# Performance work log

Measured on AMD Instinct MI355X. Metric: run time of the kernel, lower is better.

Reference implementation:

```python
import jax, jax.numpy as jnp
import numpy as np

N_NODES = 100000
N_EDGES = 1600000
N_CLASS = 26
HIDDEN = 128
K = 3  # TAGConv hops


def setup_inputs() -> dict:
    key = jax.random.key(0)
    ks = jax.random.split(key, 12)
    x = jax.random.normal(ks[0], (N_NODES, N_CLASS), dtype=jnp.float32)
    edge_index = jax.random.randint(ks[1], (2, N_EDGES), 0, N_NODES, dtype=jnp.int64)
    edge_weight = jax.random.uniform(ks[2], (N_EDGES,), dtype=jnp.float32)
    # Per-hop weights (K+1 hops incl. hop 0) for each of the 3 TAGConv layers.
    def lin(k, fan_in, fan_out):
        s = 1.0 / np.sqrt(fan_in)
        return jax.random.uniform(k, (K + 1, fan_in, fan_out), dtype=jnp.float32, minval=-s, maxval=s)
    W1 = lin(ks[3], N_CLASS, HIDDEN)
    b1 = jnp.zeros((HIDDEN,), dtype=jnp.float32)
    W2 = lin(ks[4], HIDDEN, HIDDEN)
    b2 = jnp.zeros((HIDDEN,), dtype=jnp.float32)
    W3 = lin(ks[5], HIDDEN, N_CLASS)
    b3 = jnp.zeros((N_CLASS,), dtype=jnp.float32)
    return {"x": x, "edge_index": edge_index, "edge_weight": edge_weight,
            "W1": W1, "b1": b1, "W2": W2, "b2": b2, "W3": W3, "b3": b3}


def _gcn_norm(edge_index, edge_weight, n):
    # symmetric normalization deg^-1/2 * w * deg^-1/2, no self loops (PyG TAGConv)
    row, col = edge_index[0], edge_index[1]
    deg = jax.ops.segment_sum(edge_weight, col, num_segments=n)
    dinv = jnp.where(deg > 0, jax.lax.rsqrt(jnp.maximum(deg, 1e-12)), 0.0)
    return dinv[row] * edge_weight * dinv[col]


def _tag_conv(x, row, col, norm, W, b, n):
    # out = sum_k W_k(x_k), x_0 = x, x_k = A_norm x_{k-1}
    out = x @ W[0]
    h = x
    for k in range(1, K + 1):
        h = jax.ops.segment_sum(norm[:, None] * h[row], col, num_segments=n)
        out = out + h @ W[k]
    return out + b


def reference(x, edge_index, edge_weight, W1, b1, W2, b2, W3, b3):
    n = x.shape[0]
    row, col = edge_index[0], edge_index[1]
    norm = _gcn_norm(edge_index, edge_weight, n)  # identical for all 3 layers
    h = jax.nn.elu(_tag_conv(x, row, col, norm, W1, b1, n))
    h = jax.nn.elu(_tag_conv(h, row, col, norm, W2, b2, n))
    return _tag_conv(h, row, col, norm, W3, b3, n)
```

## Files before the change

### kernel.cpp

```cpp
#include <hip/hip_runtime.h>

#define NCLS 26
#define HID 128
#define EPB 8192
#define MAXBK 512
#define BCAP 6016
typedef unsigned short ushort_t;
typedef unsigned int uint_t;
typedef unsigned long long u64;

typedef __bf16 bf16x8 __attribute__((ext_vector_type(8)));
typedef float f32x4 __attribute__((ext_vector_type(4)));
typedef unsigned int u32x4 __attribute__((ext_vector_type(4)));
typedef unsigned int u32x2 __attribute__((ext_vector_type(2)));

static __device__ __forceinline__ float b2f(ushort_t h) {
  return __uint_as_float(((uint_t)h) << 16);
}
static __device__ __forceinline__ ushort_t f2b(float f) {
  uint_t u = __float_as_uint(f);
  uint_t r = (u + 0x7fffu + ((u >> 16) & 1u)) >> 16;
  return (ushort_t)r;
}
static __device__ __forceinline__ uint_t pack2(float f0, float f1) {
  return (uint_t)f2b(f0) | ((uint_t)f2b(f1) << 16);
}
static __device__ __forceinline__ float lo16(uint_t v) { return b2f((ushort_t)(v & 0xffffu)); }
static __device__ __forceinline__ float hi16(uint_t v) { return b2f((ushort_t)(v >> 16)); }
static __device__ __forceinline__ bf16x8 ld_frag(const ushort_t* p) {
  u32x4 v = *reinterpret_cast<const u32x4*>(p);
  return __builtin_bit_cast(bf16x8, v);
}


__global__ __launch_bounds__(256) void bucket_place(
    const int* __restrict__ ei, const float* __restrict__ ew,
    int* __restrict__ gcur, u64* __restrict__ bkt, int E, int nbk) {
  __shared__ uint_t lc[MAXBK];
  __shared__ uint_t lb[MAXBK];
  int tid = threadIdx.x;
  for (int t = tid; t < nbk; t += 256) lc[t] = 0;
  __syncthreads();
  int e0 = blockIdx.x * EPB;
#pragma unroll
  for (int i = 0; i < EPB / 256; ++i) {
    int e = e0 + tid + i * 256;
    if (e < E) atomicAdd(&lc[(uint_t)ei[E + e] >> 8], 1u);
  }
  __syncthreads();
  for (int t = tid; t < nbk; t += 256) {
    uint_t c = lc[t];
    lb[t] = c ? (uint_t)t * BCAP + (uint_t)atomicAdd(&gcur[t], (int)c) : 0u;
    lc[t] = 0;
  }
  __syncthreads();
#pragma unroll
  for (int i = 0; i < EPB / 256; ++i) {
    int e = e0 + tid + i * 256;
    if (e < E) {
      uint_t r = (uint_t)ei[e];
      uint_t c = (uint_t)ei[E + e];
      uint_t b = c >> 8;
      uint_t pos = lb[b] + atomicAdd(&lc[b], 1u);
      bkt[pos] = ((u64)(r | ((c & 255u) << 24)) << 32) | (u64)__float_as_uint(ew[e]);
    }
  }
}

__global__ void scan_buckets(const int* __restrict__ gcur, int* __restrict__ mbase,
                             int nbk, int E) {
  __shared__ int s[512];
  int t = threadIdx.x;
  int v = (t < nbk) ? gcur[t] : 0;
  s[t] = v;
  __syncthreads();
  for (int off = 1; off < 512; off <<= 1) {
    int u = (t >= off) ? s[t - off] : 0;
    __syncthreads();
    s[t] += u;
    __syncthreads();
  }
  if (t < nbk) mbase[t] = s[t] - v;
  if (t == 0) mbase[nbk] = E;
}

__global__ __launch_bounds__(256) void bucket_stats(
    const u64* __restrict__ bkt, const int* __restrict__ gcur, const int* __restrict__ mbase,
    int* __restrict__ start, float* __restrict__ dinv, int n, int E) {
  int b = blockIdx.x;
  __shared__ uint_t cnt[256];
  __shared__ float deg[256];
  __shared__ int ssc[256];
  int tid = threadIdx.x;
  cnt[tid] = 0;
  deg[tid] = 0.f;
  __syncthreads();
  int fill = gcur[b];
  const u64* w = bkt + (size_t)b * BCAP;
  for (int p = tid; p < fill; p += 256) {
    u64 v = w[p];
    uint_t cl = (uint_t)(v >> 56);
    float wv = __uint_as_float((uint_t)(v & 0xffffffffULL));
    atomicAdd(&cnt[cl], 1u);
    atomicAdd(&deg[cl], wv);
  }
  __syncthreads();
  int v0 = (int)cnt[tid];
  ssc[tid] = v0;
  __syncthreads();
  for (int off = 1; off < 256; off <<= 1) {
    int u = (tid >= off) ? ssc[tid - off] : 0;
    __syncthreads();
    ssc[tid] += u;
    __syncthreads();
  }
  int node = (b << 8) + tid;
  if (node < n) {
    start[node] = mbase[b] + ssc[tid] - v0;
    float d = deg[tid];
    dinv[node] = d > 0.f ? rsqrtf(fmaxf(d, 1e-12f)) : 0.f;
  }
  if (b == 0 && tid == 0) start[n] = E;
}

__global__ __launch_bounds__(256) void bucket_emit(
    const u64* __restrict__ bkt, const int* __restrict__ gcur, const int* __restrict__ start,
    const float* __restrict__ dinv, u32x2* __restrict__ meta, int n) {
  int b = blockIdx.x;
  __shared__ uint_t lcur[256];
  int tid = threadIdx.x;
  lcur[tid] = 0;
  __syncthreads();
  int fill = gcur[b];
  const u64* w = bkt + (size_t)b * BCAP;
  for (int p = tid; p < fill; p += 256) {
    u64 v = w[p];
    uint_t hi = (uint_t)(v >> 32);
    uint_t r = hi & 0xffffffu;
    uint_t cl = hi >> 24;
    float wv = __uint_as_float((uint_t)(v & 0xffffffffULL));
    uint_t node = ((uint_t)b << 8) + cl;
    float nrm = dinv[r] * wv * dinv[node];
    uint_t slot = (uint_t)start[node] + atomicAdd(&lcur[cl], 1u);
    u32x2 m;
    m.x = r;
    m.y = __float_as_uint(nrm);
    meta[slot] = m;
  }
}

__global__ __launch_bounds__(256) void prep_misc(
    const float* __restrict__ x, uint_t* __restrict__ x32,
    const float* __restrict__ W1, ushort_t* __restrict__ Wz1,
    const float* __restrict__ W2, ushort_t* __restrict__ Wz2,
    const float* __restrict__ W3, ushort_t* __restrict__ Wz3, int n, int gconv) {
  int blk = blockIdx.x;
  int tid = threadIdx.x;
  if (blk < gconv) {
    int idx = blk * 256 + tid;
    if (idx >= n * 16) return;
    int node = idx >> 4, lane = idx & 15;
    float f0 = 0.f, f1 = 0.f;
    if (lane < 13) {
      f0 = x[node * 26 + 2 * lane];
      f1 = x[node * 26 + 2 * lane + 1];
    }
    x32[idx] = pack2(f0, f1);
  } else if (blk < gconv + 64) {
    int idx = (blk - gconv) * 256 + tid;
    int i = idx & 7, l = (idx >> 3) & 63, j = (idx >> 9) & 7, t = idx >> 12;
    int k = 8 * (l >> 4) + i;
    int col = 16 * j + (l & 15);
    float v = (k < NCLS) ? W1[((size_t)t * NCLS + k) * 128 + col] : 0.f;
    Wz1[idx] = f2b(v);
  } else if (blk < gconv + 64 + 256) {
    int idx = (blk - gconv - 64) * 256 + tid;
    int i = idx & 7, l = (idx >> 3) & 63, j = (idx >> 9) & 7, t = idx >> 12;
    int s = t >> 2, tt = t & 3;
    int k = tt * 32 + 8 * (l >> 4) + i;
    int col = 16 * j + (l & 15);
    float v = W2[((size_t)s * HID + k) * 128 + col];
    Wz2[idx] = f2b(v);
  } else {
    int idx = (blk - gconv - 64 - 256) * 256 + tid;
    int i = idx & 7, l = (idx >> 3) & 63, j = (idx >> 9) & 7, t = idx >> 12;
    int k = t * 32 + 8 * (l >> 4) + i;
    int col = 16 * j + (l & 15);
    int s = col >> 5, c = col & 31;
    float v = (c < 26) ? W3[((size_t)s * 128 + k) * 26 + c] : 0.f;
    Wz3[idx] = f2b(v);
  }
}


__global__ __launch_bounds__(256) void spmm128_bf(
    const u32x2* __restrict__ meta, const int* __restrict__ start,
    const uint_t* __restrict__ in, uint_t* __restrict__ out, int n) {
  int node = blockIdx.x * 4 + (threadIdx.x >> 6);
  int lane = threadIdx.x & 63;
  if (node >= n) return;
  int s = start[node], m = start[node + 1] - s;
  int eq = lane >> 4;
  uint_t foff = (uint_t)(lane & 15) << 4;
  const char* inb = (const char*)in;
  float a0 = 0.f, a1 = 0.f, a2 = 0.f, a3 = 0.f, a4 = 0.f, a5 = 0.f, a6 = 0.f, a7 = 0.f;
  if (m > 0) {
    int i0 = eq, i1 = 4 + eq;
    u32x2 mt0 = meta[s + (i0 < m ? i0 : m - 1)];
    u32x2 mt1 = meta[s + (i1 < m ? i1 : m - 1)];
    for (int base = 0; base < m; base += 8) {
      int p0 = base + 8 + eq, p1 = base + 12 + eq;
      u32x2 nx0 = meta[s + (p0 < m ? p0 : m - 1)];
      u32x2 nx1 = meta[s + (p1 < m ? p1 : m - 1)];
      float w0 = (base + eq < m) ? __uint_as_float(mt0.y) : 0.f;
      float w1 = (base + 4 + eq < m) ? __uint_as_float(mt1.y) : 0.f;
      u32x4 v0 = *reinterpret_cast<const u32x4*>(inb + (((uint_t)mt0.x << 8) + foff));
      u32x4 v1 = *reinterpret_cast<const u32x4*>(inb + (((uint_t)mt1.x << 8) + foff));
      a0 += w0 * lo16(v0.x); a1 += w0 * hi16(v0.x);
      a2 += w0 * lo16(v0.y); a3 += w0 * hi16(v0.y);
      a4 += w0 * lo16(v0.z); a5 += w0 * hi16(v0.z);
      a6 += w0 * lo16(v0.w); a7 += w0 * hi16(v0.w);
      a0 += w1 * lo16(v1.x); a1 += w1 * hi16(v1.x);
      a2 += w1 * lo16(v1.y); a3 += w1 * hi16(v1.y);
      a4 += w1 * lo16(v1.z); a5 += w1 * hi16(v1.z);
      a6 += w1 * lo16(v1.w); a7 += w1 * hi16(v1.w);
      mt0 = nx0;
      mt1 = nx1;
    }
  }
  a0 += __shfl_xor(a0, 16); a1 += __shfl_xor(a1, 16);
  a2 += __shfl_xor(a2, 16); a3 += __shfl_xor(a3, 16);
  a4 += __shfl_xor(a4, 16); a5 += __shfl_xor(a5, 16);
  a6 += __shfl_xor(a6, 16); a7 += __shfl_xor(a7, 16);
  a0 += __shfl_xor(a0, 32); a1 += __shfl_xor(a1, 32);
  a2 += __shfl_xor(a2, 32); a3 += __shfl_xor(a3, 32);
  a4 += __shfl_xor(a4, 32); a5 += __shfl_xor(a5, 32);
  a6 += __shfl_xor(a6, 32); a7 += __shfl_xor(a7, 32);
  if (eq == 0) {
    u32x4 o;
    o.x = pack2(a0, a1);
    o.y = pack2(a2, a3);
    o.z = pack2(a4, a5);
    o.w = pack2(a6, a7);
    *reinterpret_cast<u32x4*>(out + (size_t)node * 64 + (foff >> 2)) = o;
  }
}

__global__ __launch_bounds__(256) void spmm26_bf(
    const u32x2* __restrict__ meta, const int* __restrict__ start,
    const uint_t* __restrict__ in, const uint_t* __restrict__ add,
    uint_t* __restrict__ out, int n) {
  int node = blockIdx.x * 32 + (threadIdx.x >> 3);
  int ln = threadIdx.x & 7;
  if (node >= n) return;
  int s = start[node], m = start[node + 1] - s;
  uint_t foff = (uint_t)ln << 3;
  const char* inb = (const char*)in;
  float a0 = 0.f, a1 = 0.f, a2 = 0.f, a3 = 0.f;
  if (m > 0) {
    for (int base = 0; base < m; base += 8) {
      int j = base + ln;
      u32x2 mt = meta[s + (j < m ? j : m - 1)];
      int rr = (int)mt.x;
      float ww = (j < m) ? __uint_as_float(mt.y) : 0.f;
#pragma unroll
      for (int k = 0; k < 8; ++k) {
        uint_t r = (uint_t)__shfl(rr, k, 8);
        float wv = __shfl(ww, k, 8);
        u32x2 v = *reinterpret_cast<const u32x2*>(inb + ((r << 6) + foff));
        a0 += wv * lo16(v.x); a1 += wv * hi16(v.x);
        a2 += wv * lo16(v.y); a3 += wv * hi16(v.y);
      }
    }
  }
  if (add) {
    u32x2 v = *reinterpret_cast<const u32x2*>(add + (size_t)node * 16 + 2 * ln);
    a0 += lo16(v.x); a1 += hi16(v.x);
    a2 += lo16(v.y); a3 += hi16(v.y);
  }
  u32x2 o;
  o.x = pack2(a0, a1);
  o.y = pack2(a2, a3);
  *reinterpret_cast<u32x2*>(out + (size_t)node * 16 + 2 * ln) = o;
}

__global__ __launch_bounds__(256) void spmm26_addf(
    const u32x2* __restrict__ meta, const int* __restrict__ start,
    const uint_t* __restrict__ in, float* __restrict__ out, int n) {
  int node = blockIdx.x * 32 + (threadIdx.x >> 3);
  int ln = threadIdx.x & 7;
  if (node >= n) return;
  int s = start[node], m = start[node + 1] - s;
  uint_t foff = (uint_t)ln << 3;
  const char* inb = (const char*)in;
  float a0 = 0.f, a1 = 0.f, a2 = 0.f, a3 = 0.f;
  if (m > 0) {
    for (int base = 0; base < m; base += 8) {
      int j = base + ln;
      u32x2 mt = meta[s + (j < m ? j : m - 1)];
      int rr = (int)mt.x;
      float ww = (j < m) ? __uint_as_float(mt.y) : 0.f;
#pragma unroll
      for (int k = 0; k < 8; ++k) {
        uint_t r = (uint_t)__shfl(rr, k, 8);
        float wv = __shfl(ww, k, 8);
        u32x2 v = *reinterpret_cast<const u32x2*>(inb + ((r << 6) + foff));
        a0 += wv * lo16(v.x); a1 += wv * hi16(v.x);
        a2 += wv * lo16(v.y); a3 += wv * hi16(v.y);
      }
    }
  }
  int c0 = 4 * ln;
  if (c0 + 0 < 26) out[(size_t)node * 26 + c0 + 0] += a0;
  if (c0 + 1 < 26) out[(size_t)node * 26 + c0 + 1] += a1;
  if (c0 + 2 < 26) out[(size_t)node * 26 + c0 + 2] += a2;
  if (c0 + 3 < 26) out[(size_t)node * 26 + c0 + 3] += a3;
}

template <int KW, int NSRC, int EPI, int GROUP>
__global__ __launch_bounds__(256) void mfma_gemm(
    const ushort_t* __restrict__ A0, const ushort_t* __restrict__ A1,
    const ushort_t* __restrict__ A2, const ushort_t* __restrict__ A3,
    const ushort_t* __restrict__ Wswz, const float* __restrict__ bias,
    ushort_t* __restrict__ outb, float* __restrict__ outf, int n) {
  constexpr int KSPS = KW / 32;
  constexpr int KSTEPS = NSRC * KSPS;
  constexpr int NGROUPS = KSTEPS / GROUP;
  __shared__ ushort_t sW[GROUP * 4096];
  const int tid = threadIdx.x;
  const int w = tid >> 6;
  const int l = tid & 63;
  const int row0 = blockIdx.x * 64 + w * 16;
  const int koff = 8 * (l >> 4);
  const int arow = row0 + (l & 15);
  const int arow_c = arow < n ? arow : (n - 1);

  f32x4 acc[8];
#pragma unroll
  for (int j = 0; j < 8; ++j) acc[j] = (f32x4){0.f, 0.f, 0.f, 0.f};

  const ushort_t* const srcs[4] = {A0, A1, A2, A3};

  auto aload = [&](int t) {
    const int s = t / KSPS;
    const int tt = t - s * KSPS;
    return ld_frag(srcs[s] + (size_t)arow_c * KW + tt * 32 + koff);
  };

  bf16x8 afA[GROUP], afB[GROUP];
#pragma unroll
  for (int c = 0; c < GROUP; ++c) afA[c] = aload(c);
  u32x4 gw[2 * GROUP];
#pragma unroll
  for (int c = 0; c < GROUP; ++c) {
    const ushort_t* p = Wswz + (size_t)c * 4096 + tid * 8;
    gw[2 * c] = *reinterpret_cast<const u32x4*>(p);
    gw[2 * c + 1] = *reinterpret_cast<const u32x4*>(p + 2048);
  }

#pragma unroll
  for (int g = 0; g < NGROUPS; ++g) {
    __syncthreads();
#pragma unroll
    for (int c = 0; c < GROUP; ++c) {
      *reinterpret_cast<u32x4*>(sW + c * 4096 + tid * 8) = gw[2 * c];
      *reinterpret_cast<u32x4*>(sW + c * 4096 + tid * 8 + 2048) = gw[2 * c + 1];
    }
    if (g + 1 < NGROUPS) {
#pragma unroll
      for (int c = 0; c < GROUP; ++c) {
        const ushort_t* p = Wswz + (size_t)(g + 1) * GROUP * 4096 + (size_t)c * 4096 + tid * 8;
        gw[2 * c] = *reinterpret_cast<const u32x4*>(p);
        gw[2 * c + 1] = *reinterpret_cast<const u32x4*>(p + 2048);
      }
#pragma unroll
      for (int c = 0; c < GROUP; ++c) {
        if (g & 1)
          afA[c] = aload((g + 1) * GROUP + c);
        else
          afB[c] = aload((g + 1) * GROUP + c);
      }
    }
    __syncthreads();
#pragma unroll
    for (int tg = 0; tg < GROUP; ++tg) {
      bf16x8 af = (g & 1) ? afB[tg] : afA[tg];
      const ushort_t* wp = sW + tg * 4096 + l * 8;
#pragma unroll
      for (int j = 0; j < 8; ++j) {
        bf16x8 bfr = ld_frag(wp + j * 64 * 8);
        acc[j] = __builtin_amdgcn_mfma_f32_16x16x32_bf16(af, bfr, acc[j], 0, 0, 0);
      }
    }
  }

  const int ccol = l & 15;
  const int crow0 = row0 + 4 * (l >> 4);
#pragma unroll
  for (int j = 0; j < 8; ++j) {
    if (EPI == 0) {
      int col = 16 * j + ccol;
      float bi = bias[col];
#pragma unroll
      for (int r = 0; r < 4; ++r) {
        int row = crow0 + r;
        if (row >= n) continue;
        float v = acc[j][r] + bi;
        v = v > 0.f ? v : (__expf(v) - 1.f);
        outb[(size_t)row * 128 + col] = f2b(v);
      }
    } else {
      int slot = j >> 1;
      int c = 16 * (j & 1) + ccol;
#pragma unroll
      for (int r = 0; r < 4; ++r) {
        int row = crow0 + r;
        if (row >= n) continue;
        float v = acc[j][r];
        if (slot == 0) {
          if (c < 26) outf[(size_t)row * 26 + c] = v + bias[c];
        } else {
          outb[((size_t)(slot - 1) * n + row) * 32 + c] = f2b(v);
        }
      }
    }
  }
}


extern "C" void kernel_launch(void* const* d_in, const int* in_sizes, int n_in,
                              void* d_out, int out_size, void* d_ws, size_t ws_size,
                              hipStream_t stream) {
  const float* x  = (const float*)d_in[0];
  const int*   ei = (const int*)d_in[1];
  const float* ew = (const float*)d_in[2];
  const float* W1 = (const float*)d_in[3];
  const float* b1 = (const float*)d_in[4];
  const float* W2 = (const float*)d_in[5];
  const float* b2 = (const float*)d_in[6];
  const float* W3 = (const float*)d_in[7];
  const float* b3 = (const float*)d_in[8];
  float* out = (float*)d_out;

  const int n = in_sizes[0] / NCLS;
  const int E = in_sizes[2];
  const int nbk = (n + 255) >> 8;

  char* w = (char*)d_ws;
  auto alloc = [&](size_t bytes) {
    char* p = w;
    w += (bytes + 255) / 256 * 256;
    return p;
  };
  uint_t* H0 = (uint_t*)alloc((size_t)n * 64 * 4);
  uint_t* P1 = (uint_t*)alloc((size_t)n * 64 * 4);
  uint_t* P2 = (uint_t*)alloc((size_t)n * 64 * 4);
  uint_t* P3 = (uint_t*)alloc((size_t)n * 64 * 4);
  uint_t* H1 = (uint_t*)alloc((size_t)n * 64 * 4);
  uint_t* x32 = (uint_t*)alloc((size_t)n * 16 * 4);
  uint_t* q1  = (uint_t*)alloc((size_t)n * 16 * 4);
  uint_t* q2  = (uint_t*)alloc((size_t)n * 16 * 4);
  uint_t* q3  = (uint_t*)alloc((size_t)n * 16 * 4);
  uint_t* zb  = (uint_t*)alloc((size_t)n * 48 * 4);
  ushort_t* Wz1 = (ushort_t*)alloc(4 * 4096 * 2);
  ushort_t* Wz2 = (ushort_t*)alloc(16 * 4096 * 2);
  ushort_t* Wz3 = (ushort_t*)alloc(4 * 4096 * 2);
  u64*   bkt  = (u64*)zb;
  u32x2* meta = (u32x2*)alloc((size_t)E * 8);
  int*   start = (int*)alloc((size_t)(n + 1) * 4);
  float* dinv  = (float*)alloc((size_t)n * 4);
  int*   gcur  = (int*)alloc(MAXBK * 4);
  int*   mbase = (int*)alloc((MAXBK + 1) * 4);

  const int ab = (E + EPB - 1) / EPB;
  const int gconv = (n * 16 + 255) / 256;

  prep_misc<<<gconv + 64 + 256 + 64, 256, 0, stream>>>(x, x32, W1, Wz1, W2, Wz2, W3, Wz3,
                                                       n, gconv);

  hipMemsetAsync(gcur, 0, MAXBK * 4, stream);
  bucket_place<<<ab, 256, 0, stream>>>(ei, ew, gcur, bkt, E, nbk);
  scan_buckets<<<1, 512, 0, stream>>>(gcur, mbase, nbk, E);
  bucket_stats<<<nbk, 256, 0, stream>>>(bkt, gcur, mbase, start, dinv, n, E);
  bucket_emit<<<nbk, 256, 0, stream>>>(bkt, gcur, start, dinv, meta, n);

  const int g128 = (n + 3) / 4;
  const int g26  = (n + 31) / 32;
  const int gg   = (n + 63) / 64;

  spmm26_bf<<<g26, 256, 0, stream>>>(meta, start, x32, nullptr, q1, n);
  spmm26_bf<<<g26, 256, 0, stream>>>(meta, start, q1, nullptr, q2, n);
  spmm26_bf<<<g26, 256, 0, stream>>>(meta, start, q2, nullptr, q3, n);
  mfma_gemm<32, 4, 0, 4><<<gg, 256, 0, stream>>>(
      (const ushort_t*)x32, (const ushort_t*)q1, (const ushort_t*)q2, (const ushort_t*)q3,
      Wz1, b1, (ushort_t*)H0, nullptr, n);

  spmm128_bf<<<g128, 256, 0, stream>>>(meta, start, H0, P1, n);
  spmm128_bf<<<g128, 256, 0, stream>>>(meta, start, P1, P2, n);
  spmm128_bf<<<g128, 256, 0, stream>>>(meta, start, P2, P3, n);
  mfma_gemm<128, 4, 0, 4><<<gg, 256, 0, stream>>>(
      (const ushort_t*)H0, (const ushort_t*)P1, (const ushort_t*)P2, (const ushort_t*)P3,
      Wz2, b2, (ushort_t*)H1, nullptr, n);

  mfma_gemm<128, 1, 1, 4><<<gg, 256, 0, stream>>>(
      (const ushort_t*)H1, (const ushort_t*)H1, (const ushort_t*)H1, (const ushort_t*)H1,
      Wz3, b3, (ushort_t*)zb, out, n);

  uint_t* z1 = zb;
  uint_t* z2 = zb + (size_t)n * 16;
  uint_t* z3 = zb + (size_t)n * 32;
  spmm26_bf<<<g26, 256, 0, stream>>>(meta, start, z3, z2, q1, n);
  spmm26_bf<<<g26, 256, 0, stream>>>(meta, start, q1, z1, q2, n);
  spmm26_addf<<<g26, 256, 0, stream>>>(meta, start, q2, out, n);
}
```

Before: 458.1 us.

## Slice feature matrices into 16-column planes and pack edge metadata into 32 bits

Stores all node-feature matrices as column slices of 16 bf16 values, so each row slice is 32 bytes, and rewrites the SpMM kernels so each block handles one slice for a group of nodes, processing two nodes per wavefront. Edge metadata is compressed to a single 32-bit word: a 17-bit source index plus a 15-bit bf16 weight with the sign bit dropped. The GEMM loads and epilogues are updated to read and write the sliced layout. The aim is to improve cache locality of the random gathers, since each slice pass touches a smaller working set, and to halve metadata traffic. The cost is lower weight precision, a node count limited to 17 bits, and metadata being re-read once per slice.

```diff
diff --git a/kernel.cpp b/kernel.cpp
--- a/kernel.cpp
+++ b/kernel.cpp
@@ -125,7 +125,7 @@
 
 __global__ __launch_bounds__(256) void bucket_emit(
     const u64* __restrict__ bkt, const int* __restrict__ gcur, const int* __restrict__ start,
-    const float* __restrict__ dinv, u32x2* __restrict__ meta, int n) {
+    const float* __restrict__ dinv, uint_t* __restrict__ meta, int n) {
   int b = blockIdx.x;
   __shared__ uint_t lcur[256];
   int tid = threadIdx.x;
@@ -142,10 +142,7 @@
     uint_t node = ((uint_t)b << 8) + cl;
     float nrm = dinv[r] * wv * dinv[node];
     uint_t slot = (uint_t)start[node] + atomicAdd(&lcur[cl], 1u);
-    u32x2 m;
-    m.x = r;
-    m.y = __float_as_uint(nrm);
-    meta[slot] = m;
+    meta[slot] = (((uint_t)f2b(nrm) & 0x7FFFu) << 17) | r;
   }
 }
 
@@ -165,7 +162,7 @@
       f0 = x[node * 26 + 2 * lane];
       f1 = x[node * 26 + 2 * lane + 1];
     }
-    x32[idx] = pack2(f0, f1);
+    x32[((size_t)(lane >> 3) * n + node) * 8 + (lane & 7)] = pack2(f0, f1);
   } else if (blk < gconv + 64) {
     int idx = (blk - gconv) * 256 + tid;
     int i = idx & 7, l = (idx >> 3) & 63, j = (idx >> 9) & 7, t = idx >> 12;
@@ -192,129 +189,122 @@
   }
 }
 
-
-__global__ __launch_bounds__(256) void spmm128_bf(
-    const u32x2* __restrict__ meta, const int* __restrict__ start,
-    const uint_t* __restrict__ in, uint_t* __restrict__ out, int n) {
-  int node = blockIdx.x * 4 + (threadIdx.x >> 6);
-  int lane = threadIdx.x & 63;
-  if (node >= n) return;
-  int s = start[node], m = start[node + 1] - s;
-  int eq = lane >> 4;
-  uint_t foff = (uint_t)(lane & 15) << 4;
-  const char* inb = (const char*)in;
-  float a0 = 0.f, a1 = 0.f, a2 = 0.f, a3 = 0.f, a4 = 0.f, a5 = 0.f, a6 = 0.f, a7 = 0.f;
-  if (m > 0) {
-    int i0 = eq, i1 = 4 + eq;
-    u32x2 mt0 = meta[s + (i0 < m ? i0 : m - 1)];
-    u32x2 mt1 = meta[s + (i1 < m ? i1 : m - 1)];
-    for (int base = 0; base < m; base += 8) {
-      int p0 = base + 8 + eq, p1 = base + 12 + eq;
-      u32x2 nx0 = meta[s + (p0 < m ? p0 : m - 1)];
-      u32x2 nx1 = meta[s + (p1 < m ? p1 : m - 1)];
-      float w0 = (base + eq < m) ? __uint_as_float(mt0.y) : 0.f;
-      float w1 = (base + 4 + eq < m) ? __uint_as_float(mt1.y) : 0.f;
-      u32x4 v0 = *reinterpret_cast<const u32x4*>(inb + (((uint_t)mt0.x << 8) + foff));
-      u32x4 v1 = *reinterpret_cast<const u32x4*>(inb + (((uint_t)mt1.x << 8) + foff));
-      a0 += w0 * lo16(v0.x); a1 += w0 * hi16(v0.x);
-      a2 += w0 * lo16(v0.y); a3 += w0 * hi16(v0.y);
-      a4 += w0 * lo16(v0.z); a5 += w0 * hi16(v0.z);
-      a6 += w0 * lo16(v0.w); a7 += w0 * hi16(v0.w);
-      a0 += w1 * lo16(v1.x); a1 += w1 * hi16(v1.x);
-      a2 += w1 * lo16(v1.y); a3 += w1 * hi16(v1.y);
-      a4 += w1 * lo16(v1.z); a5 += w1 * hi16(v1.z);
-      a6 += w1 * lo16(v1.w); a7 += w1 * hi16(v1.w);
-      mt0 = nx0;
-      mt1 = nx1;
-    }
-  }
-  a0 += __shfl_xor(a0, 16); a1 += __shfl_xor(a1, 16);
-  a2 += __shfl_xor(a2, 16); a3 += __shfl_xor(a3, 16);
-  a4 += __shfl_xor(a4, 16); a5 += __shfl_xor(a5, 16);
-  a6 += __shfl_xor(a6, 16); a7 += __shfl_xor(a7, 16);
-  a0 += __shfl_xor(a0, 32); a1 += __shfl_xor(a1, 32);
-  a2 += __shfl_xor(a2, 32); a3 += __shfl_xor(a3, 32);
-  a4 += __shfl_xor(a4, 32); a5 += __shfl_xor(a5, 32);
-  a6 += __shfl_xor(a6, 32); a7 += __shfl_xor(a7, 32);
-  if (eq == 0) {
-    u32x4 o;
-    o.x = pack2(a0, a1);
-    o.y = pack2(a2, a3);
-    o.z = pack2(a4, a5);
-    o.w = pack2(a6, a7);
-    *reinterpret_cast<u32x4*>(out + (size_t)node * 64 + (foff >> 2)) = o;
-  }
-}
-
-__global__ __launch_bounds__(256) void spmm26_bf(
-    const u32x2* __restrict__ meta, const int* __restrict__ start,
+template <int NSLOG, int NPW>
+__global__ __launch_bounds__(256) void spmm_sl(
+    const uint_t* __restrict__ umeta, const int* __restrict__ start,
     const uint_t* __restrict__ in, const uint_t* __restrict__ add,
     uint_t* __restrict__ out, int n) {
-  int node = blockIdx.x * 32 + (threadIdx.x >> 3);
-  int ln = threadIdx.x & 7;
-  if (node >= n) return;
-  int s = start[node], m = start[node + 1] - s;
-  uint_t foff = (uint_t)ln << 3;
-  const char* inb = (const char*)in;
-  float a0 = 0.f, a1 = 0.f, a2 = 0.f, a3 = 0.f;
-  if (m > 0) {
-    for (int base = 0; base < m; base += 8) {
-      int j = base + ln;
-      u32x2 mt = meta[s + (j < m ? j : m - 1)];
-      int rr = (int)mt.x;
-      float ww = (j < m) ? __uint_as_float(mt.y) : 0.f;
-#pragma unroll
-      for (int k = 0; k < 8; ++k) {
-        uint_t r = (uint_t)__shfl(rr, k, 8);
-        float wv = __shfl(ww, k, 8);
-        u32x2 v = *reinterpret_cast<const u32x2*>(inb + ((r << 6) + foff));
-        a0 += wv * lo16(v.x); a1 += wv * hi16(v.x);
-        a2 += wv * lo16(v.y); a3 += wv * hi16(v.y);
-      }
-    }
-  }
-  if (add) {
-    u32x2 v = *reinterpret_cast<const u32x2*>(add + (size_t)node * 16 + 2 * ln);
-    a0 += lo16(v.x); a1 += hi16(v.x);
-    a2 += lo16(v.y); a3 += hi16(v.y);
-  }
-  u32x2 o;
-  o.x = pack2(a0, a1);
-  o.y = pack2(a2, a3);
-  *reinterpret_cast<u32x2*>(out + (size_t)node * 16 + 2 * ln) = o;
-}
-
-__global__ __launch_bounds__(256) void spmm26_addf(
-    const u32x2* __restrict__ meta, const int* __restrict__ start,
+  constexpr int NS = 1 << NSLOG;
+  const int bid = blockIdx.x;
+  const int sl = bid & (NS - 1);
+  const int wid = threadIdx.x >> 6;
+  const int lane = threadIdx.x & 63;
+  const int eg = lane >> 2, fl = lane & 3;
+  const size_t slb = (size_t)sl * ((size_t)n * 8);
+  const uint_t* inS = in + slb;
+  const int node0 = (bid >> NSLOG) * (4 * NPW) + wid * NPW;
+
+#pragma unroll
+  for (int nn = 0; nn < NPW; nn += 2) {
+    int nodeA = node0 + nn;
+    int nodeB = node0 + nn + 1;
+    if (nodeA >= n) return;
+    bool hasB = nodeB < n;
+    int sA = start[nodeA], mA = start[nodeA + 1] - sA;
+    int sB = hasB ? start[nodeB] : sA;
+    int mB = hasB ? start[nodeB + 1] - sB : 0;
+    float a0 = 0.f, a1 = 0.f, a2 = 0.f, a3 = 0.f;
+    float b0 = 0.f, b1 = 0.f, b2 = 0.f, b3 = 0.f;
+    int mmax = mA > mB ? mA : mB;
+    for (int base = 0; base < mmax; base += 16) {
+      int e = base + eg;
+      int ciA = e < mA ? e : (mA > 0 ? mA - 1 : 0);
+      int ciB = e < mB ? e : (mB > 0 ? mB - 1 : 0);
+      uint_t mvA = umeta[sA + ciA];
+      uint_t mvB = umeta[sB + ciB];
+      float wA = (e < mA) ? __uint_as_float((mvA >> 17) << 16) : 0.f;
+      float wB = (e < mB) ? __uint_as_float((mvB >> 17) << 16) : 0.f;
+      u32x2 vA = *reinterpret_cast<const u32x2*>(inS + (mvA & 0x1FFFFu) * 8 + fl * 2);
+      u32x2 vB = *reinterpret_cast<const u32x2*>(inS + (mvB & 0x1FFFFu) * 8 + fl * 2);
+      a0 += wA * lo16(vA.x); a1 += wA * hi16(vA.x);
+      a2 += wA * lo16(vA.y); a3 += wA * hi16(vA.y);
+      b0 += wB * lo16(vB.x); b1 += wB * hi16(vB.x);
+      b2 += wB * lo16(vB.y); b3 += wB * hi16(vB.y);
+    }
+#pragma unroll
+    for (int st = 4; st <= 32; st <<= 1) {
+      a0 += __shfl_xor(a0, st); a1 += __shfl_xor(a1, st);
+      a2 += __shfl_xor(a2, st); a3 += __shfl_xor(a3, st);
+      b0 += __shfl_xor(b0, st); b1 += __shfl_xor(b1, st);
+      b2 += __shfl_xor(b2, st); b3 += __shfl_xor(b3, st);
+    }
+    if (lane < 4) {
+      size_t oA = slb + (size_t)nodeA * 8 + fl * 2;
+      if (add) {
+        u32x2 av = *reinterpret_cast<const u32x2*>(add + oA);
+        a0 += lo16(av.x); a1 += hi16(av.x);
+        a2 += lo16(av.y); a3 += hi16(av.y);
+      }
+      u32x2 ov;
+      ov.x = pack2(a0, a1);
+      ov.y = pack2(a2, a3);
+      *reinterpret_cast<u32x2*>(out + oA) = ov;
+      if (hasB) {
+        size_t oB = slb + (size_t)nodeB * 8 + fl * 2;
+        if (add) {
+          u32x2 av = *reinterpret_cast<const u32x2*>(add + oB);
+          b0 += lo16(av.x); b1 += hi16(av.x);
+          b2 += lo16(av.y); b3 += hi16(av.y);
+        }
+        u32x2 ov2;
+        ov2.x = pack2(b0, b1);
+        ov2.y = pack2(b2, b3);
+        *reinterpret_cast<u32x2*>(out + oB) = ov2;
+      }
+    }
+  }
+}
+
+template <int NPW>
+__global__ __launch_bounds__(256) void spmm_addf_sl(
+    const uint_t* __restrict__ umeta, const int* __restrict__ start,
     const uint_t* __restrict__ in, float* __restrict__ out, int n) {
-  int node = blockIdx.x * 32 + (threadIdx.x >> 3);
-  int ln = threadIdx.x & 7;
-  if (node >= n) return;
-  int s = start[node], m = start[node + 1] - s;
-  uint_t foff = (uint_t)ln << 3;
-  const char* inb = (const char*)in;
-  float a0 = 0.f, a1 = 0.f, a2 = 0.f, a3 = 0.f;
-  if (m > 0) {
-    for (int base = 0; base < m; base += 8) {
-      int j = base + ln;
-      u32x2 mt = meta[s + (j < m ? j : m - 1)];
-      int rr = (int)mt.x;
-      float ww = (j < m) ? __uint_as_float(mt.y) : 0.f;
-#pragma unroll
-      for (int k = 0; k < 8; ++k) {
-        uint_t r = (uint_t)__shfl(rr, k, 8);
-        float wv = __shfl(ww, k, 8);
-        u32x2 v = *reinterpret_cast<const u32x2*>(inb + ((r << 6) + foff));
-        a0 += wv * lo16(v.x); a1 += wv * hi16(v.x);
-        a2 += wv * lo16(v.y); a3 += wv * hi16(v.y);
-      }
-    }
-  }
-  int c0 = 4 * ln;
-  if (c0 + 0 < 26) out[(size_t)node * 26 + c0 + 0] += a0;
-  if (c0 + 1 < 26) out[(size_t)node * 26 + c0 + 1] += a1;
-  if (c0 + 2 < 26) out[(size_t)node * 26 + c0 + 2] += a2;
-  if (c0 + 3 < 26) out[(size_t)node * 26 + c0 + 3] += a3;
+  const int bid = blockIdx.x;
+  const int sl = bid & 1;
+  const int wid = threadIdx.x >> 6;
+  const int lane = threadIdx.x & 63;
+  const int eg = lane >> 2, fl = lane & 3;
+  const size_t slb = (size_t)sl * ((size_t)n * 8);
+  const uint_t* inS = in + slb;
+  const int node0 = (bid >> 1) * (4 * NPW) + wid * NPW;
+
+#pragma unroll
+  for (int nn = 0; nn < NPW; ++nn) {
+    int node = node0 + nn;
+    if (node >= n) return;
+    int s = start[node], m = start[node + 1] - s;
+    float a0 = 0.f, a1 = 0.f, a2 = 0.f, a3 = 0.f;
+    for (int base = 0; base < m; base += 16) {
+      int e = base + eg;
+      uint_t mv = umeta[s + (e < m ? e : m - 1)];
+      float w = (e < m) ? __uint_as_float((mv >> 17) << 16) : 0.f;
+      u32x2 v = *reinterpret_cast<const u32x2*>(inS + (mv & 0x1FFFFu) * 8 + fl * 2);
+      a0 += w * lo16(v.x); a1 += w * hi16(v.x);
+      a2 += w * lo16(v.y); a3 += w * hi16(v.y);
+    }
+#pragma unroll
+    for (int st = 4; st <= 32; st <<= 1) {
+      a0 += __shfl_xor(a0, st); a1 += __shfl_xor(a1, st);
+      a2 += __shfl_xor(a2, st); a3 += __shfl_xor(a3, st);
+    }
+    if (lane < 4) {
+      int c0 = sl * 16 + fl * 4;
+      if (c0 + 0 < 26) out[(size_t)node * 26 + c0 + 0] += a0;
+      if (c0 + 1 < 26) out[(size_t)node * 26 + c0 + 1] += a1;
+      if (c0 + 2 < 26) out[(size_t)node * 26 + c0 + 2] += a2;
+      if (c0 + 3 < 26) out[(size_t)node * 26 + c0 + 3] += a3;
+    }
+  }
 }
 
 template <int KW, int NSRC, int EPI, int GROUP>
@@ -344,7 +334,8 @@
   auto aload = [&](int t) {
     const int s = t / KSPS;
     const int tt = t - s * KSPS;
-    return ld_frag(srcs[s] + (size_t)arow_c * KW + tt * 32 + koff);
+    const int k0 = tt * 32 + koff;
+    return ld_frag(srcs[s] + ((size_t)(k0 >> 4) * n + arow_c) * 16 + (k0 & 15));
   };
 
   bf16x8 afA[GROUP], afB[GROUP];
@@ -399,15 +390,14 @@
 #pragma unroll
   for (int j = 0; j < 8; ++j) {
     if (EPI == 0) {
-      int col = 16 * j + ccol;
-      float bi = bias[col];
+      float bi = bias[16 * j + ccol];
 #pragma unroll
       for (int r = 0; r < 4; ++r) {
         int row = crow0 + r;
         if (row >= n) continue;
         float v = acc[j][r] + bi;
         v = v > 0.f ? v : (__expf(v) - 1.f);
-        outb[(size_t)row * 128 + col] = f2b(v);
+        outb[((size_t)j * n + row) * 16 + ccol] = f2b(v);
       }
     } else {
       int slot = j >> 1;
@@ -420,7 +410,7 @@
         if (slot == 0) {
           if (c < 26) outf[(size_t)row * 26 + c] = v + bias[c];
         } else {
-          outb[((size_t)(slot - 1) * n + row) * 32 + c] = f2b(v);
+          outb[((size_t)((slot - 1) * 2 + (j & 1)) * n + row) * 16 + ccol] = f2b(v);
         }
       }
     }
@@ -466,7 +456,7 @@
   ushort_t* Wz2 = (ushort_t*)alloc(16 * 4096 * 2);
   ushort_t* Wz3 = (ushort_t*)alloc(4 * 4096 * 2);
   u64*   bkt  = (u64*)zb;
-  u32x2* meta = (u32x2*)alloc((size_t)E * 8);
+  uint_t* meta = (uint_t*)alloc((size_t)E * 4);
   int*   start = (int*)alloc((size_t)(n + 1) * 4);
   float* dinv  = (float*)alloc((size_t)n * 4);
   int*   gcur  = (int*)alloc(MAXBK * 4);
@@ -484,20 +474,21 @@
   bucket_stats<<<nbk, 256, 0, stream>>>(bkt, gcur, mbase, start, dinv, n, E);
   bucket_emit<<<nbk, 256, 0, stream>>>(bkt, gcur, start, dinv, meta, n);
 
-  const int g128 = (n + 3) / 4;
-  const int g26  = (n + 31) / 32;
-  const int gg   = (n + 63) / 64;
-
-  spmm26_bf<<<g26, 256, 0, stream>>>(meta, start, x32, nullptr, q1, n);
-  spmm26_bf<<<g26, 256, 0, stream>>>(meta, start, q1, nullptr, q2, n);
-  spmm26_bf<<<g26, 256, 0, stream>>>(meta, start, q2, nullptr, q3, n);
+  const int gblk = (n + 31) / 32;
+  const int g128sl = gblk * 8;
+  const int g26sl  = gblk * 2;
+  const int gg     = (n + 63) / 64;
+
+  spmm_sl<1, 8><<<g26sl, 256, 0, stream>>>(meta, start, x32, nullptr, q1, n);
+  spmm_sl<1, 8><<<g26sl, 256, 0, stream>>>(meta, start, q1, nullptr, q2, n);
+  spmm_sl<1, 8><<<g26sl, 256, 0, stream>>>(meta, start, q2, nullptr, q3, n);
   mfma_gemm<32, 4, 0, 4><<<gg, 256, 0, stream>>>(
       (const ushort_t*)x32, (const ushort_t*)q1, (const ushort_t*)q2, (const ushort_t*)q3,
       Wz1, b1, (ushort_t*)H0, nullptr, n);
 
-  spmm128_bf<<<g128, 256, 0, stream>>>(meta, start, H0, P1, n);
-  spmm128_bf<<<g128, 256, 0, stream>>>(meta, start, P1, P2, n);
-  spmm128_bf<<<g128, 256, 0, stream>>>(meta, start, P2, P3, n);
+  spmm_sl<3, 8><<<g128sl, 256, 0, stream>>>(meta, start, H0, nullptr, P1, n);
+  spmm_sl<3, 8><<<g128sl, 256, 0, stream>>>(meta, start, P1, nullptr, P2, n);
+  spmm_sl<3, 8><<<g128sl, 256, 0, stream>>>(meta, start, P2, nullptr, P3, n);
   mfma_gemm<128, 4, 0, 4><<<gg, 256, 0, stream>>>(
       (const ushort_t*)H0, (const ushort_t*)P1, (const ushort_t*)P2, (const ushort_t*)P3,
       Wz2, b2, (ushort_t*)H1, nullptr, n);
@@ -509,7 +500,7 @@
   uint_t* z1 = zb;
   uint_t* z2 = zb + (size_t)n * 16;
   uint_t* z3 = zb + (size_t)n * 32;
-  spmm26_bf<<<g26, 256, 0, stream>>>(meta, start, z3, z2, q1, n);
-  spmm26_bf<<<g26, 256, 0, stream>>>(meta, start, q1, z1, q2, n);
-  spmm26_addf<<<g26, 256, 0, stream>>>(meta, start, q2, out, n);
-}
+  spmm_sl<1, 8><<<g26sl, 256, 0, stream>>>(meta, start, z3, z2, q1, n);
+  spmm_sl<1, 8><<<g26sl, 256, 0, stream>>>(meta, start, q1, z1, q2, n);
+  spmm_addf_sl<8><<<g26sl, 256, 0, stream>>>(meta, start, q2, out, n);
+}
```

Result: slower. 856.3 us (+86.9%).
